# Kernel tuning notes

Measured on AMD Instinct MI355X. Metric: run time of the kernel, lower is better.

## Reference

```python
import jax, jax.numpy as jnp
import numpy as np


def setup_inputs() -> dict:
    key = jax.random.key(0)
    ks = jax.random.split(key, 16)
    B, C, H, W = 2, 64, 512, 512
    Nl, Nr = 100000, 20000

    def lin(k, fan_in, fan_out):
        kw, kb = jax.random.split(k)
        bound = 1.0 / np.sqrt(fan_in)
        w = jax.random.uniform(kw, (fan_in, fan_out), jnp.float32, -bound, bound)
        b = jax.random.uniform(kb, (fan_out,), jnp.float32, -bound, bound)
        return w, b

    w_lin, b_lin = lin(ks[0], 128, 64)
    w1, b1 = lin(ks[1], 128, 64)
    w2, b2 = lin(ks[2], 64, 32)
    w3, b3 = lin(ks[3], 32, 16)
    w4, b4 = lin(ks[4], 16, 1)

    return {
        "pc0_map": jax.random.normal(ks[5], (B, C, H, W), jnp.float32),
        "pc1_map": jax.random.normal(ks[6], (B, C, H, W), jnp.float32),
        "flow_map": jax.random.normal(ks[7], (B, C, H, W), jnp.float32),
        "lidar_coords": jax.random.randint(ks[8], (B, Nl, 3), 0, 512).astype(jnp.int64),
        "radar_coords": jax.random.randint(ks[9], (B, Nr, 3), 0, 512).astype(jnp.int64),
        "w_lin": w_lin, "b_lin": b_lin,
        "w1": w1, "b1": b1, "w2": w2, "b2": b2,
        "w3": w3, "b3": b3, "w4": w4, "b4": b4,
    }


def reference(pc0_map, pc1_map, flow_map, lidar_coords, radar_coords,
              w_lin, b_lin, w1, b1, w2, b2, w3, b3, w4, b4):
    gelu = lambda x: jax.nn.gelu(x, approximate=False)  # torch nn.GELU default (erf)

    def seg_single(p0, p1, fl, lc, rc):
        # lc: [Nl,3], rc: [Nr,3]; cat(lidar, radar) for all three maps
        coords = jnp.concatenate([lc, rc], axis=0)        # [N,3]
        r, c = coords[:, 1], coords[:, 2]
        f0 = p0[:, r, c].T                                # [N,64]
        f1 = p1[:, r, c].T                                # [N,64]
        ff = fl[:, r, c].T                                # [N,64]
        pc = jnp.concatenate([f0, f1], axis=1) @ w_lin + b_lin   # [N,64]
        h = jnp.concatenate([pc, ff], axis=1)             # [N,128]
        h = gelu(h @ w1 + b1)
        h = gelu(h @ w2 + b2)
        h = gelu(h @ w3 + b3)
        s = jax.nn.sigmoid(h @ w4 + b4)                   # [N,1]
        return s[:, 0]

    # [B, Nl+Nr] stacked (original returns a per-batch list; fixed N lets us stack)
    return jax.vmap(seg_single)(pc0_map, pc1_map, flow_map, lidar_coords, radar_coords)
```

## Files before the change

### kernel.cpp

```cpp
#include <hip/hip_runtime.h>
#include <math.h>

#define NPTS 120000
#define NLID 100000
#define NRAD 20000
#define NTOT (2 * NPTS)
#define MAPW 512
#define MAPHW (512 * 512)

typedef short sh8 __attribute__((ext_vector_type(8)));
typedef float f32x4 __attribute__((ext_vector_type(4)));
typedef unsigned short u16;
typedef unsigned int u32;

#define GSTR 264
#define H1S 72
#define H2S 40
#define H3S 24
#define HWAVE (16 * (H1S + H2S + H3S))

__device__ __forceinline__ float gelu_f(float x) {
    return 0.5f * x * (1.0f + erff(x * 0.7071067811865476f));
}
__device__ __forceinline__ u16 f2bf(float f) {
    unsigned int u = __float_as_uint(f);
    return (u16)((u + 0x7FFFu + ((u >> 16) & 1u)) >> 16);
}
__device__ __forceinline__ float bf2f(u16 h) {
    return __uint_as_float((unsigned int)h << 16);
}

__global__ void wprep_kernel(const float* __restrict__ w_lin, const float* __restrict__ b_lin,
                             const float* __restrict__ w1, const float* __restrict__ b1,
                             const float* __restrict__ w2, const float* __restrict__ w3,
                             u16* __restrict__ wfrag1, u16* __restrict__ wfrag2,
                             u16* __restrict__ wfrag3, float* __restrict__ b_eff) {
    int e = blockIdx.x * blockDim.x + threadIdx.x;
    if (e < 12288) {
        int fi = e >> 9, r = e & 511, lane = r >> 3, j = r & 7;
        int kk = fi >> 2, nt = fi & 3;
        int k = kk * 32 + (lane >> 4) * 8 + j;
        int n = nt * 16 + (lane & 15);
        float val;
        if (k < 128) {
            float s = 0.f;
            for (int jj = 0; jj < 64; jj++) s += w_lin[k * 64 + jj] * w1[jj * 64 + n];
            val = s;
        } else {
            val = w1[(k - 64) * 64 + n];
        }
        wfrag1[e] = f2bf(val);
    } else if (e < 12288 + 2048) {
        int e2 = e - 12288;
        int fi = e2 >> 9, lane = (e2 >> 3) & 63, j = e2 & 7;
        int kk = fi >> 1, nt = fi & 1;
        int k = kk * 32 + (lane >> 4) * 8 + j;
        int n = nt * 16 + (lane & 15);
        wfrag2[e2] = f2bf(w2[k * 32 + n]);
    } else if (e < 12288 + 2048 + 512) {
        int e3 = e - 12288 - 2048;
        int lane = e3 >> 3, j = e3 & 7;
        int k = (lane >> 4) * 8 + j;
        int n = lane & 15;
        wfrag3[e3] = f2bf(w3[k * 16 + n]);
    } else if (e < 12288 + 2048 + 512 + 64) {
        int n = e - 12288 - 2048 - 512;
        float s = b1[n];
        for (int jj = 0; jj < 64; jj++) s += b_lin[jj] * w1[jj * 64 + n];
        b_eff[n] = s;
    }
}

__global__ __launch_bounds__(256) void fbseg_dense_kernel(
    const float* __restrict__ p0, const float* __restrict__ p1,
    const float* __restrict__ fl,
    const u16* __restrict__ wfrag1, const u16* __restrict__ wfrag2,
    const u16* __restrict__ wfrag3, const float* __restrict__ b_eff,
    const float* __restrict__ b2, const float* __restrict__ b3,
    const float* __restrict__ w4, const float* __restrict__ b4,
    float* __restrict__ score)
{
    __shared__ __align__(16) float smem[48 * GSTR];

    const int tid = threadIdx.x;
    const int wv = tid >> 6;
    const int lane = tid & 63;

    const int nb = blockIdx.x;
    const int b  = nb >> 12;
    const int r  = (nb & 4095) >> 3;
    const int c0 = (nb & 7) << 6;

    {
        const size_t off = (size_t)b * ((size_t)64 * MAPHW)
                         + (size_t)r * MAPW + (size_t)c0
                         + (size_t)(lane >> 4) * MAPHW
                         + (size_t)((lane & 15) * 4);
        const float* bases[3] = {p0 + off, p1 + off, fl + off};
        #pragma unroll
        for (int m = 0; m < 3; m++) {
            #pragma unroll
            for (int u = 0; u < 4; u++) {
                const int g = u * 4 + wv;
                const int G = __builtin_amdgcn_readfirstlane(m * 16 + g);
                const float* gp = bases[m] + (size_t)(g * 4) * MAPHW;
                __builtin_amdgcn_global_load_lds(
                    (const __attribute__((address_space(1))) u32*)gp,
                    (__attribute__((address_space(3))) u32*)(&smem[G * GSTR]),
                    16, 0, 0);
            }
        }
    }
    __syncthreads();

    const int m0 = wv * 16;
    const int lr = lane & 15;
    const int lq = lane >> 4;
    const int col = m0 + lr;

    f32x4 acc1[4] = {};
    #pragma unroll
    for (int kk = 0; kk < 6; kk++) {
        sh8 a;
        u16* ap = (u16*)&a;
        #pragma unroll
        for (int j = 0; j < 8; j++) {
            const int k = kk * 32 + lq * 8 + j;
            ap[j] = f2bf(smem[(k >> 2) * GSTR + (k & 3) * 64 + col]);
        }
        #pragma unroll
        for (int nt = 0; nt < 4; nt++) {
            sh8 bfr = *(const sh8*)(wfrag1 + ((kk * 4 + nt) * 64 + lane) * 8);
            acc1[nt] = __builtin_amdgcn_mfma_f32_16x16x32_bf16(a, bfr, acc1[nt], 0, 0, 0);
        }
    }
    __syncthreads();

    u16* Hbase = (u16*)smem + wv * HWAVE;
    u16* H1w = Hbase;
    u16* H2w = Hbase + 16 * H1S;
    u16* H3w = Hbase + 16 * H1S + 16 * H2S;

    #pragma unroll
    for (int nt = 0; nt < 4; nt++) {
        const int n = nt * 16 + lr;
        const float bias = b_eff[n];
        #pragma unroll
        for (int rg = 0; rg < 4; rg++) {
            const int row = lq * 4 + rg;
            H1w[row * H1S + n] = f2bf(gelu_f(acc1[nt][rg] + bias));
        }
    }

    f32x4 acc2[2] = {};
    #pragma unroll
    for (int kk = 0; kk < 2; kk++) {
        sh8 a = *(const sh8*)&H1w[lr * H1S + kk * 32 + lq * 8];
        #pragma unroll
        for (int nt = 0; nt < 2; nt++) {
            sh8 bfr = *(const sh8*)(wfrag2 + ((kk * 2 + nt) * 64 + lane) * 8);
            acc2[nt] = __builtin_amdgcn_mfma_f32_16x16x32_bf16(a, bfr, acc2[nt], 0, 0, 0);
        }
    }
    #pragma unroll
    for (int nt = 0; nt < 2; nt++) {
        const int n = nt * 16 + lr;
        const float bias = b2[n];
        #pragma unroll
        for (int rg = 0; rg < 4; rg++) {
            const int row = lq * 4 + rg;
            H2w[row * H2S + n] = f2bf(gelu_f(acc2[nt][rg] + bias));
        }
    }

    f32x4 acc3 = {};
    {
        sh8 a = *(const sh8*)&H2w[lr * H2S + lq * 8];
        sh8 bfr = *(const sh8*)(wfrag3 + lane * 8);
        acc3 = __builtin_amdgcn_mfma_f32_16x16x32_bf16(a, bfr, acc3, 0, 0, 0);
    }
    {
        const float bias = b3[lr];
        #pragma unroll
        for (int rg = 0; rg < 4; rg++) {
            const int row = lq * 4 + rg;
            H3w[row * H3S + lr] = f2bf(gelu_f(acc3[rg] + bias));
        }
    }

    if (lane < 16) {
        float s = b4[0];
        #pragma unroll
        for (int k = 0; k < 16; k++) s = fmaf(bf2f(H3w[lane * H3S + k]), w4[k], s);
        score[(size_t)b * MAPHW + (size_t)r * MAPW + (size_t)(c0 + m0 + lane)] =
            1.0f / (1.0f + expf(-s));
    }
}

__global__ void lookup_kernel(const int* __restrict__ lidar, const int* __restrict__ radar,
                              const float* __restrict__ score, float* __restrict__ out) {
    int p = blockIdx.x * blockDim.x + threadIdx.x;
    if (p >= NTOT) return;
    int b = p / NPTS;
    int i = p - b * NPTS;
    int r, c;
    if (i < NLID) {
        const int* cd = lidar + (size_t)(b * NLID + i) * 3;
        r = cd[1]; c = cd[2];
    } else {
        const int* cd = radar + (size_t)(b * NRAD + (i - NLID)) * 3;
        r = cd[1]; c = cd[2];
    }
    out[p] = score[(size_t)b * MAPHW + (size_t)r * MAPW + (size_t)c];
}

extern "C" void kernel_launch(void* const* d_in, const int* in_sizes, int n_in,
                              void* d_out, int out_size, void* d_ws, size_t ws_size,
                              hipStream_t stream) {
    const float* p0    = (const float*)d_in[0];
    const float* p1    = (const float*)d_in[1];
    const float* fl    = (const float*)d_in[2];
    const int*   lidar = (const int*)d_in[3];
    const int*   radar = (const int*)d_in[4];
    const float* w_lin = (const float*)d_in[5];
    const float* b_lin = (const float*)d_in[6];
    const float* w1    = (const float*)d_in[7];
    const float* b1    = (const float*)d_in[8];
    const float* w2    = (const float*)d_in[9];
    const float* b2    = (const float*)d_in[10];
    const float* w3    = (const float*)d_in[11];
    const float* b3    = (const float*)d_in[12];
    const float* w4    = (const float*)d_in[13];
    const float* b4    = (const float*)d_in[14];
    float* out = (float*)d_out;

    char* ws = (char*)d_ws;
    float* score = (float*)ws;
    char* wbase  = ws + (size_t)2 * MAPHW * sizeof(float);
    u16*  wfrag1 = (u16*)wbase;
    u16*  wfrag2 = (u16*)(wbase + 12288 * 2);
    u16*  wfrag3 = (u16*)(wbase + (12288 + 2048) * 2);
    float* b_eff = (float*)(wbase + (12288 + 2048 + 512) * 2);

    hipLaunchKernelGGL(wprep_kernel, dim3((14912 + 255) / 256), dim3(256), 0, stream,
                       w_lin, b_lin, w1, b1, w2, w3, wfrag1, wfrag2, wfrag3, b_eff);
    hipLaunchKernelGGL(fbseg_dense_kernel, dim3(8192), dim3(256), 0, stream,
                       p0, p1, fl, wfrag1, wfrag2, wfrag3, b_eff, b2, b3, w4, b4, score);
    hipLaunchKernelGGL(lookup_kernel, dim3((NTOT + 255) / 256), dim3(256), 0, stream,
                       lidar, radar, score, out);
}
```

Before: 407.9 us.

## Convert dense MLP kernel to persistent grid with split-half software-pipelined loads

The dense scoring kernel now launches a fixed grid of 768 persistent blocks that loop over the 8192 tiles. Each tile's 48 channel groups are loaded into shared memory in two halves, and the next tile's loads are issued while the current tile is still in its layer-one MFMAs and tail layers. The hidden-activation scratch reuses the second input half, and bias values are hoisted into registers outside the loop. The aim is to hide global-to-LDS load latency and cut per-block launch overhead, at the cost of manual vmcnt/lgkmcnt waits and barriers whose ordering must be exactly right.

```diff
diff --git a/kernel.cpp b/kernel.cpp
--- a/kernel.cpp
+++ b/kernel.cpp
@@ -7,6 +7,8 @@
 #define NTOT (2 * NPTS)
 #define MAPW 512
 #define MAPHW (512 * 512)
+#define NTILES 8192
+#define PGRID 768
 
 typedef short sh8 __attribute__((ext_vector_type(8)));
 typedef float f32x4 __attribute__((ext_vector_type(4)));
@@ -18,6 +20,9 @@
 #define H2S 40
 #define H3S 24
 #define HWAVE (16 * (H1S + H2S + H3S))
+
+#define MEMFENCE() asm volatile("" ::: "memory")
+#define BARRIER() do { MEMFENCE(); __builtin_amdgcn_s_barrier(); MEMFENCE(); } while (0)
 
 __device__ __forceinline__ float gelu_f(float x) {
     return 0.5f * x * (1.0f + erff(x * 0.7071067811865476f));
@@ -71,6 +76,33 @@
     }
 }
 
+__device__ __forceinline__ void issue_half(int h, int nb, int lane, int wv, float* smem,
+                                           const float* __restrict__ p0,
+                                           const float* __restrict__ p1,
+                                           const float* __restrict__ fl) {
+    const int b  = nb >> 12;
+    const int r  = (nb & 4095) >> 3;
+    const int c0 = (nb & 7) << 6;
+    const size_t off = (size_t)b * ((size_t)64 * MAPHW)
+                     + (size_t)r * MAPW + (size_t)c0
+                     + (size_t)(lane >> 4) * MAPHW
+                     + (size_t)((lane & 15) * 4);
+    #pragma unroll
+    for (int s = 0; s < 6; s++) {
+        const int idx = h * 6 + s;
+        const int m = idx >> 2;
+        const int u = idx & 3;
+        const int g = u * 4 + wv;
+        const int G = __builtin_amdgcn_readfirstlane(m * 16 + g);
+        const float* base = (m == 0) ? p0 : ((m == 1) ? p1 : fl);
+        const float* gp = base + off + (size_t)(g * 4) * MAPHW;
+        __builtin_amdgcn_global_load_lds(
+            (const __attribute__((address_space(1))) u32*)gp,
+            (__attribute__((address_space(3))) u32*)(&smem[G * GSTR]),
+            16, 0, 0);
+    }
+}
+
 __global__ __launch_bounds__(256) void fbseg_dense_kernel(
     const float* __restrict__ p0, const float* __restrict__ p1,
     const float* __restrict__ fl,
@@ -82,118 +114,146 @@
 {
     __shared__ __align__(16) float smem[48 * GSTR];
 
-    const int tid = threadIdx.x;
-    const int wv = tid >> 6;
+    const int tid  = threadIdx.x;
+    const int wv   = tid >> 6;
     const int lane = tid & 63;
-
-    const int nb = blockIdx.x;
-    const int b  = nb >> 12;
-    const int r  = (nb & 4095) >> 3;
-    const int c0 = (nb & 7) << 6;
-
-    {
-        const size_t off = (size_t)b * ((size_t)64 * MAPHW)
-                         + (size_t)r * MAPW + (size_t)c0
-                         + (size_t)(lane >> 4) * MAPHW
-                         + (size_t)((lane & 15) * 4);
-        const float* bases[3] = {p0 + off, p1 + off, fl + off};
-        #pragma unroll
-        for (int m = 0; m < 3; m++) {
-            #pragma unroll
-            for (int u = 0; u < 4; u++) {
-                const int g = u * 4 + wv;
-                const int G = __builtin_amdgcn_readfirstlane(m * 16 + g);
-                const float* gp = bases[m] + (size_t)(g * 4) * MAPHW;
-                __builtin_amdgcn_global_load_lds(
-                    (const __attribute__((address_space(1))) u32*)gp,
-                    (__attribute__((address_space(3))) u32*)(&smem[G * GSTR]),
-                    16, 0, 0);
-            }
-        }
-    }
-    __syncthreads();
-
-    const int m0 = wv * 16;
-    const int lr = lane & 15;
-    const int lq = lane >> 4;
-    const int col = m0 + lr;
-
-    f32x4 acc1[4] = {};
-    #pragma unroll
-    for (int kk = 0; kk < 6; kk++) {
-        sh8 a;
-        u16* ap = (u16*)&a;
-        #pragma unroll
-        for (int j = 0; j < 8; j++) {
-            const int k = kk * 32 + lq * 8 + j;
-            ap[j] = f2bf(smem[(k >> 2) * GSTR + (k & 3) * 64 + col]);
-        }
-        #pragma unroll
-        for (int nt = 0; nt < 4; nt++) {
-            sh8 bfr = *(const sh8*)(wfrag1 + ((kk * 4 + nt) * 64 + lane) * 8);
-            acc1[nt] = __builtin_amdgcn_mfma_f32_16x16x32_bf16(a, bfr, acc1[nt], 0, 0, 0);
-        }
-    }
-    __syncthreads();
-
-    u16* Hbase = (u16*)smem + wv * HWAVE;
+    const int lr   = lane & 15;
+    const int lq   = lane >> 4;
+    const int m0w  = wv * 16;
+    const int col  = m0w + lr;
+
+    u16* Hbase = (u16*)(smem + 24 * GSTR) + wv * HWAVE;
     u16* H1w = Hbase;
     u16* H2w = Hbase + 16 * H1S;
     u16* H3w = Hbase + 16 * H1S + 16 * H2S;
 
-    #pragma unroll
-    for (int nt = 0; nt < 4; nt++) {
-        const int n = nt * 16 + lr;
-        const float bias = b_eff[n];
+    const float beffr0 = b_eff[lr], beffr1 = b_eff[16 + lr],
+                beffr2 = b_eff[32 + lr], beffr3 = b_eff[48 + lr];
+    const float b2r0 = b2[lr], b2r1 = b2[16 + lr];
+    const float b3r = b3[lr];
+    const float b4r = b4[0];
+
+    int nb = blockIdx.x;
+    issue_half(0, nb, lane, wv, smem, p0, p1, fl);
+    issue_half(1, nb, lane, wv, smem, p0, p1, fl);
+
+    while (true) {
+        const int nbn = nb + PGRID;
+        const bool more = (nbn < NTILES);
+
+        asm volatile("s_waitcnt vmcnt(6)" ::: "memory");
+        BARRIER();
+
+        f32x4 acc1[4] = {};
+        #pragma unroll
+        for (int kk = 0; kk < 3; kk++) {
+            sh8 a;
+            u16* ap = (u16*)&a;
+            #pragma unroll
+            for (int j = 0; j < 8; j++) {
+                const int k = kk * 32 + lq * 8 + j;
+                ap[j] = f2bf(smem[(k >> 2) * GSTR + (k & 3) * 64 + col]);
+            }
+            #pragma unroll
+            for (int nt = 0; nt < 4; nt++) {
+                sh8 bfr = *(const sh8*)(wfrag1 + ((kk * 4 + nt) * 64 + lane) * 8);
+                acc1[nt] = __builtin_amdgcn_mfma_f32_16x16x32_bf16(a, bfr, acc1[nt], 0, 0, 0);
+            }
+        }
+
+        asm volatile("s_waitcnt lgkmcnt(0)" ::: "memory");
+        BARRIER();
+        if (more) {
+            issue_half(0, nbn, lane, wv, smem, p0, p1, fl);
+            asm volatile("s_waitcnt vmcnt(6)" ::: "memory");
+        } else {
+            asm volatile("s_waitcnt vmcnt(0)" ::: "memory");
+        }
+        BARRIER();
+
+        #pragma unroll
+        for (int kk = 3; kk < 6; kk++) {
+            sh8 a;
+            u16* ap = (u16*)&a;
+            #pragma unroll
+            for (int j = 0; j < 8; j++) {
+                const int k = kk * 32 + lq * 8 + j;
+                ap[j] = f2bf(smem[(k >> 2) * GSTR + (k & 3) * 64 + col]);
+            }
+            #pragma unroll
+            for (int nt = 0; nt < 4; nt++) {
+                sh8 bfr = *(const sh8*)(wfrag1 + ((kk * 4 + nt) * 64 + lane) * 8);
+                acc1[nt] = __builtin_amdgcn_mfma_f32_16x16x32_bf16(a, bfr, acc1[nt], 0, 0, 0);
+            }
+        }
+
+        asm volatile("s_waitcnt lgkmcnt(0)" ::: "memory");
+        BARRIER();
+
+        {
+            const float bias[4] = {beffr0, beffr1, beffr2, beffr3};
+            #pragma unroll
+            for (int nt = 0; nt < 4; nt++) {
+                const int n = nt * 16 + lr;
+                #pragma unroll
+                for (int rg = 0; rg < 4; rg++) {
+                    const int row = lq * 4 + rg;
+                    H1w[row * H1S + n] = f2bf(gelu_f(acc1[nt][rg] + bias[nt]));
+                }
+            }
+        }
+
+        f32x4 acc2[2] = {};
+        #pragma unroll
+        for (int kk = 0; kk < 2; kk++) {
+            sh8 a = *(const sh8*)&H1w[lr * H1S + kk * 32 + lq * 8];
+            #pragma unroll
+            for (int nt = 0; nt < 2; nt++) {
+                sh8 bfr = *(const sh8*)(wfrag2 + ((kk * 2 + nt) * 64 + lane) * 8);
+                acc2[nt] = __builtin_amdgcn_mfma_f32_16x16x32_bf16(a, bfr, acc2[nt], 0, 0, 0);
+            }
+        }
+        {
+            const float bias[2] = {b2r0, b2r1};
+            #pragma unroll
+            for (int nt = 0; nt < 2; nt++) {
+                const int n = nt * 16 + lr;
+                #pragma unroll
+                for (int rg = 0; rg < 4; rg++) {
+                    const int row = lq * 4 + rg;
+                    H2w[row * H2S + n] = f2bf(gelu_f(acc2[nt][rg] + bias[nt]));
+                }
+            }
+        }
+
+        f32x4 acc3 = {};
+        {
+            sh8 a = *(const sh8*)&H2w[lr * H2S + lq * 8];
+            sh8 bfr = *(const sh8*)(wfrag3 + lane * 8);
+            acc3 = __builtin_amdgcn_mfma_f32_16x16x32_bf16(a, bfr, acc3, 0, 0, 0);
+        }
         #pragma unroll
         for (int rg = 0; rg < 4; rg++) {
             const int row = lq * 4 + rg;
-            H1w[row * H1S + n] = f2bf(gelu_f(acc1[nt][rg] + bias));
-        }
-    }
-
-    f32x4 acc2[2] = {};
-    #pragma unroll
-    for (int kk = 0; kk < 2; kk++) {
-        sh8 a = *(const sh8*)&H1w[lr * H1S + kk * 32 + lq * 8];
-        #pragma unroll
-        for (int nt = 0; nt < 2; nt++) {
-            sh8 bfr = *(const sh8*)(wfrag2 + ((kk * 2 + nt) * 64 + lane) * 8);
-            acc2[nt] = __builtin_amdgcn_mfma_f32_16x16x32_bf16(a, bfr, acc2[nt], 0, 0, 0);
-        }
-    }
-    #pragma unroll
-    for (int nt = 0; nt < 2; nt++) {
-        const int n = nt * 16 + lr;
-        const float bias = b2[n];
-        #pragma unroll
-        for (int rg = 0; rg < 4; rg++) {
-            const int row = lq * 4 + rg;
-            H2w[row * H2S + n] = f2bf(gelu_f(acc2[nt][rg] + bias));
-        }
-    }
-
-    f32x4 acc3 = {};
-    {
-        sh8 a = *(const sh8*)&H2w[lr * H2S + lq * 8];
-        sh8 bfr = *(const sh8*)(wfrag3 + lane * 8);
-        acc3 = __builtin_amdgcn_mfma_f32_16x16x32_bf16(a, bfr, acc3, 0, 0, 0);
-    }
-    {
-        const float bias = b3[lr];
-        #pragma unroll
-        for (int rg = 0; rg < 4; rg++) {
-            const int row = lq * 4 + rg;
-            H3w[row * H3S + lr] = f2bf(gelu_f(acc3[rg] + bias));
-        }
-    }
-
-    if (lane < 16) {
-        float s = b4[0];
-        #pragma unroll
-        for (int k = 0; k < 16; k++) s = fmaf(bf2f(H3w[lane * H3S + k]), w4[k], s);
-        score[(size_t)b * MAPHW + (size_t)r * MAPW + (size_t)(c0 + m0 + lane)] =
-            1.0f / (1.0f + expf(-s));
+            H3w[row * H3S + lr] = f2bf(gelu_f(acc3[rg] + b3r));
+        }
+
+        if (lane < 16) {
+            float s = b4r;
+            #pragma unroll
+            for (int k = 0; k < 16; k++) s = fmaf(bf2f(H3w[lane * H3S + k]), w4[k], s);
+            const int b  = nb >> 12;
+            const int r  = (nb & 4095) >> 3;
+            const int c0 = (nb & 7) << 6;
+            score[(size_t)b * MAPHW + (size_t)r * MAPW + (size_t)(c0 + m0w + lane)] =
+                1.0f / (1.0f + expf(-s));
+        }
+
+        asm volatile("s_waitcnt lgkmcnt(0)" ::: "memory");
+        BARRIER();
+        if (!more) break;
+        issue_half(1, nbn, lane, wv, smem, p0, p1, fl);
+        nb = nbn;
     }
 }
 
@@ -244,7 +304,7 @@
 
     hipLaunchKernelGGL(wprep_kernel, dim3((14912 + 255) / 256), dim3(256), 0, stream,
                        w_lin, b_lin, w1, b1, w2, w3, wfrag1, wfrag2, wfrag3, b_eff);
-    hipLaunchKernelGGL(fbseg_dense_kernel, dim3(8192), dim3(256), 0, stream,
+    hipLaunchKernelGGL(fbseg_dense_kernel, dim3(PGRID), dim3(256), 0, stream,
                        p0, p1, fl, wfrag1, wfrag2, wfrag3, b_eff, b2, b3, w4, b4, score);
     hipLaunchKernelGGL(lookup_kernel, dim3((NTOT + 255) / 256), dim3(256), 0, stream,
                        lidar, radar, score, out);
```

New measurement: 432.0 us. 5.9% more time.
